# Kernel optimization log

Hardware: AMD Instinct MI355X
Metric: run time of the kernel (lower is better)

Reference implementation:

```python
import jax, jax.numpy as jnp
import numpy as np


def setup_inputs() -> dict:
    key = jax.random.key(0)
    ks = jax.random.split(key, 7)
    B, L, S, H, E, M = 4, 2048, 2048, 8, 64, 4
    return {
        "queries": jax.random.normal(ks[0], (B, L, H, E), dtype=jnp.float32),
        "keys": jax.random.normal(ks[1], (B, S, H, E), dtype=jnp.float32),
        "values": jax.random.normal(ks[2], (B, S, H, E), dtype=jnp.float32),
        "query_omegas": jax.random.normal(ks[3], (B, L, H, M), dtype=jnp.float32),
        "query_thetas": jax.random.normal(ks[4], (B, L, H, M), dtype=jnp.float32),
        "key_omegas": jax.random.normal(ks[5], (B, S, H, M), dtype=jnp.float32),
        "key_thetas": jax.random.normal(ks[6], (B, S, H, M), dtype=jnp.float32),
    }


def _rotate(x, cos, sin, signs):
    # x: (B,T,H,E) split into 4 quaternion components of size E/4
    # cos/sin: (B,T,H,M); output: (B,T,H,M,E) matching torch.cat of einsum pairs
    x0, x1, x2, x3 = jnp.split(x, 4, axis=-1)  # each (B,T,H,E/4)
    c = cos[..., None]  # (B,T,H,M,1)
    s = sin[..., None]
    (a0, b0), (a1, b1), (a2, b2), (a3, b3) = signs
    parts = [
        x0[:, :, :, None, :] * c + a0 * b0[0][:, :, :, None, :] * s if False else None
    ]
    # explicit faithful construction below
    return None


def reference(queries, keys, values, query_omegas, query_thetas, key_omegas, key_thetas):
    B, L, H, E = queries.shape
    S = keys.shape[1]
    M = query_omegas.shape[-1]

    q_pos = (jnp.arange(L, dtype=queries.dtype) / L).reshape(L, 1, 1)
    k_pos = (jnp.arange(S, dtype=keys.dtype) / S).reshape(S, 1, 1)

    Qa = query_omegas * q_pos + query_thetas  # (B,L,H,M)
    Ka = key_omegas * k_pos + key_thetas      # (B,S,H,M)
    Qc, Qs = jnp.cos(Qa)[..., None], jnp.sin(Qa)[..., None]  # (B,L,H,M,1)
    Kc, Ks = jnp.cos(Ka)[..., None], jnp.sin(Ka)[..., None]  # (B,S,H,M,1)

    q0, q1, q2, q3 = [q[:, :, :, None, :] for q in jnp.split(queries, 4, axis=-1)]  # (B,L,H,1,E/4)
    k0, k1, k2, k3 = [k[:, :, :, None, :] for k in jnp.split(keys, 4, axis=-1)]     # (B,S,H,1,E/4)

    Q_rot = jnp.concatenate([
        q0 * Qc - q1 * Qs,
        q1 * Qc + q0 * Qs,
        q2 * Qc + q3 * Qs,
        q3 * Qc - q2 * Qs,
    ], axis=-1)  # (B,L,H,M,E)
    K_rot = jnp.concatenate([
        k0 * Kc - k2 * Ks,
        k1 * Kc - k3 * Ks,
        k2 * Kc + k0 * Ks,
        k3 * Kc + k1 * Ks,
    ], axis=-1)  # (B,S,H,M,E)

    scale = 1.0 / np.sqrt(E)
    scores = jnp.einsum('blhme,bshme->bhls', Q_rot, K_rot) / M  # (B,H,L,S)
    A = jax.nn.softmax(scale * scores, axis=-1)
    V = jnp.einsum('bhls,bshd->blhd', A, values)  # (B,L,H,E)
    return V
```

## Files before the change

kernel.cpp:

```cpp
#include <hip/hip_runtime.h>
#include <math.h>


#define B_ 4
#define L_ 2048
#define S_ 2048
#define H_ 8
#define E_ 64
#define M_ 4
#define QBLK 256
#define NTH 512

typedef _Float16 f16x4 __attribute__((ext_vector_type(4)));
typedef _Float16 f16x8 __attribute__((ext_vector_type(8)));
typedef __fp16 fp16x2 __attribute__((ext_vector_type(2)));
typedef float f32x4 __attribute__((ext_vector_type(4)));

union H4U { f16x4 h; fp16x2 p[2]; };
union H8U { f16x8 h; fp16x2 p[4]; };
union F4U { float4 v; float f[4]; };

__device__ __forceinline__ f16x4 cvt4(float x, float y, float z, float w) {
    H4U r;
    r.p[0] = __builtin_amdgcn_cvt_pkrtz(x, y);
    r.p[1] = __builtin_amdgcn_cvt_pkrtz(z, w);
    return r.h;
}
__device__ __forceinline__ f16x8 cvt8(const float* v) {
    H8U r;
#pragma unroll
    for (int i = 0; i < 4; ++i) r.p[i] = __builtin_amdgcn_cvt_pkrtz(v[2 * i], v[2 * i + 1]);
    return r.h;
}

__global__ __launch_bounds__(NTH)
void qattn7(const float* __restrict__ qp, const float* __restrict__ kp,
            const float* __restrict__ vp,
            const float* __restrict__ qo, const float* __restrict__ qt,
            const float* __restrict__ ko, const float* __restrict__ ktt,
            float* __restrict__ out)
{
    const int bid0 = blockIdx.x;
    const int nl = (bid0 & 7) * 32 + (bid0 >> 3);
    const int l0 = (nl & 7) * QBLK;
    const int h  = (nl >> 3) & 7;
    const int b  = nl >> 6;
    const int t  = threadIdx.x;
    const int wv   = t >> 6;
    const int lane = t & 63;
    const int quad = lane >> 4;
    const int nn   = lane & 15;

    __shared__ __align__(16) unsigned char smem[73728];
    _Float16 (*krot)[256] = reinterpret_cast<_Float16 (*)[256]>(smem);
    _Float16 (*vts)[64]   = reinterpret_cast<_Float16 (*)[64]>(smem + 32768);
    _Float16 (*pss)[64]   = reinterpret_cast<_Float16 (*)[64]>(smem + 40960);
    float (*qstage)[64] = reinterpret_cast<float (*)[64]>(smem);
    float (*qtrc)[4] = reinterpret_cast<float (*)[4]>(smem + 65536);
    float (*qtrs)[4] = reinterpret_cast<float (*)[4]>(smem + 65536 + 4096);

    const float* kb0 = kp  + ((size_t)((b * S_) * H_ + h)) * E_;
    const float* vb0 = vp  + ((size_t)((b * S_) * H_ + h)) * E_;
    const float* kob = ko  + ((size_t)((b * S_) * H_ + h)) * M_;
    const float* ktb = ktt + ((size_t)((b * S_) * H_ + h)) * M_;

    const int key_r = t >> 3;
    const int ccr   = (t >> 1) & 3;
    const int eh    = t & 1;
    const int swz   = key_r & 7;
    const int tt = t & 255;
    const int kg = tt >> 4;
    const int eg = tt & 15;

    F4U kA[2], kB[2], omR, thR, vv[4];
    auto LOAD = [&](int s0) {
        const float* kr = kb0 + (size_t)(s0 + key_r) * (H_ * E_);
        kA[0].v = *(const float4*)(kr + ccr * 16 + eh * 8);
        kA[1].v = *(const float4*)(kr + ccr * 16 + eh * 8 + 4);
        kB[0].v = *(const float4*)(kr + (ccr ^ 2) * 16 + eh * 8);
        kB[1].v = *(const float4*)(kr + (ccr ^ 2) * 16 + eh * 8 + 4);
        omR.v = *(const float4*)(kob + (size_t)(s0 + key_r) * (H_ * M_));
        thR.v = *(const float4*)(ktb + (size_t)(s0 + key_r) * (H_ * M_));
        if (t >= 256) {
#pragma unroll
            for (int j = 0; j < 4; ++j)
                vv[j].v = *(const float4*)(vb0 + (size_t)(s0 + kg * 4 + j) * (H_ * E_) + eg * 4);
        }
    };
    LOAD(0);

    f16x8 qa[2][8];
    {
        const float* qb = qp + ((size_t)((b * L_ + l0) * H_ + h)) * E_;
#pragma unroll
        for (int i = 0; i < 8; ++i) {
            int idx = t + NTH * i;
            int row = idx >> 4, c16 = idx & 15;
            *(float4*)&qstage[row][c16 * 4] =
                *(const float4*)(qb + (size_t)row * (H_ * E_) + c16 * 4);
        }
        {
            int row = t >> 1, m0 = (t & 1) * 2;
#pragma unroll
            for (int dm = 0; dm < 2; ++dm) {
                int m = m0 + dm;
                size_t off = (size_t)((b * L_ + l0 + row) * H_ + h) * M_ + m;
                float ang = qo[off] * ((float)(l0 + row) * (1.0f / L_)) + qt[off];
                float sv, cv;
                __sincosf(ang, &sv, &cv);
                qtrc[row][m] = cv;
                qtrs[row][m] = sv;
            }
        }
        __syncthreads();
#pragma unroll
        for (int set = 0; set < 2; ++set) {
            const int row = wv * 32 + set * 16 + nn;
            const int i0 = (quad & 1) * 8;
            float sl0[8], sl1[8], sl2[8], sl3[8];
            *(float4*)&sl0[0] = *(float4*)&qstage[row][ 0 + i0];
            *(float4*)&sl0[4] = *(float4*)&qstage[row][ 4 + i0];
            *(float4*)&sl1[0] = *(float4*)&qstage[row][16 + i0];
            *(float4*)&sl1[4] = *(float4*)&qstage[row][20 + i0];
            *(float4*)&sl2[0] = *(float4*)&qstage[row][32 + i0];
            *(float4*)&sl2[4] = *(float4*)&qstage[row][36 + i0];
            *(float4*)&sl3[0] = *(float4*)&qstage[row][48 + i0];
            *(float4*)&sl3[4] = *(float4*)&qstage[row][52 + i0];
            const bool hiC = (quad & 2) != 0;
            float aE[8], bE[8], aO[8], bO[8];
#pragma unroll
            for (int j = 0; j < 8; ++j) {
                aE[j] = hiC ? sl1[j] : sl0[j];
                bE[j] = hiC ? sl0[j] : sl1[j];
                aO[j] = hiC ? sl3[j] : sl2[j];
                bO[j] = hiC ? sl2[j] : sl3[j];
            }
            F4U qc4, qs4;
            qc4.v = *(float4*)&qtrc[row][0];
            qs4.v = *(float4*)&qtrs[row][0];
            const float SC = 0.04508422017f;
#pragma unroll
            for (int m = 0; m < 4; ++m) {
                float cm = qc4.f[m] * SC;
                float sm = qs4.f[m] * SC;
                float sE = hiC ? sm : -sm;
                float vE[8], vO[8];
#pragma unroll
                for (int j = 0; j < 8; ++j) {
                    vE[j] = fmaf(bE[j], sE, aE[j] * cm);
                    vO[j] = fmaf(bO[j], -sE, aO[j] * cm);
                }
                qa[set][2 * m]     = cvt8(vE);
                qa[set][2 * m + 1] = cvt8(vO);
            }
        }
        __syncthreads();
    }

    f32x4 Oacc[2][4] = {{{0,0,0,0},{0,0,0,0},{0,0,0,0},{0,0,0,0}},
                        {{0,0,0,0},{0,0,0,0},{0,0,0,0},{0,0,0,0}}};
    float mrow[2] = {-1e30f, -1e30f};
    float lrow[2] = {0.f, 0.f};
    const int xr0 = nn & 7;
    const int swq = (nn & 7) ^ (nn >> 3);

    for (int s0 = 0; s0 < S_; s0 += 64) {
        {
            float af[8], bf[8];
#pragma unroll
            for (int i2 = 0; i2 < 4; ++i2) {
                af[i2]     = kA[0].f[i2];
                af[4 + i2] = kA[1].f[i2];
                bf[i2]     = kB[0].f[i2];
                bf[4 + i2] = kB[1].f[i2];
            }
            float posk = (float)(s0 + key_r) * (1.0f / S_);
            float kcv[4], ksv[4];
#pragma unroll
            for (int m = 0; m < 4; ++m) {
                float ang = omR.f[m] * posk + thR.f[m];
                __sincosf(ang, &ksv[m], &kcv[m]);
            }
            const float sgn = (ccr >= 2) ? 1.f : -1.f;
#pragma unroll
            for (int m = 0; m < 4; ++m) {
                float cm = kcv[m], sm = ksv[m] * sgn;
                float vals[8];
#pragma unroll
                for (int i = 0; i < 8; ++i)
                    vals[i] = fmaf(bf[i], sm, af[i] * cm);
                int ch = (m * 8) | ((ccr * 2 + eh) ^ swz);
                *(f16x8*)&krot[key_r][ch * 8] = cvt8(vals);
            }
        }
        if (t >= 256) {
#pragma unroll
            for (int e = 0; e < 4; ++e) {
                int row = eg * 4 + e;
                int ch = ((kg >> 1) ^ (row & 7));
                *(f16x4*)&vts[row][ch * 8 + (kg & 1) * 4] =
                    cvt4(vv[0].f[e], vv[1].f[e], vv[2].f[e], vv[3].f[e]);
            }
        }
        if (s0 + 64 < S_) LOAD(s0 + 64);
        __syncthreads();

        float sc[2][4][4];
#pragma unroll
        for (int kt2 = 0; kt2 < 4; ++kt2) {
            const int keyb = kt2 * 16 + nn;
            f32x4 acc0 = {0, 0, 0, 0}, acc1 = {0, 0, 0, 0};
#pragma unroll
            for (int ks = 0; ks < 8; ++ks) {
                f16x8 bK = *(const f16x8*)&krot[keyb][((ks * 4 + quad) ^ xr0) * 8];
                acc0 = __builtin_amdgcn_mfma_f32_16x16x32_f16(bK, qa[0][ks], acc0, 0, 0, 0);
                acc1 = __builtin_amdgcn_mfma_f32_16x16x32_f16(bK, qa[1][ks], acc1, 0, 0, 0);
            }
#pragma unroll
            for (int r = 0; r < 4; ++r) { sc[0][kt2][r] = acc0[r]; sc[1][kt2][r] = acc1[r]; }
        }

#pragma unroll
        for (int set = 0; set < 2; ++set) {
            const int rowq = wv * 32 + set * 16 + nn;
            float m01 = fmaxf(fmaxf(sc[set][0][0], sc[set][0][1]), fmaxf(sc[set][0][2], sc[set][0][3]));
            float m23 = fmaxf(fmaxf(sc[set][1][0], sc[set][1][1]), fmaxf(sc[set][1][2], sc[set][1][3]));
            float m45 = fmaxf(fmaxf(sc[set][2][0], sc[set][2][1]), fmaxf(sc[set][2][2], sc[set][2][3]));
            float m67 = fmaxf(fmaxf(sc[set][3][0], sc[set][3][1]), fmaxf(sc[set][3][2], sc[set][3][3]));
            float tm = fmaxf(fmaxf(m01, m23), fmaxf(m45, m67));
            tm = fmaxf(tm, __shfl_xor(tm, 16));
            tm = fmaxf(tm, __shfl_xor(tm, 32));

            if (__any(tm > mrow[set] + 8.0f)) {
                float mnew  = fmaxf(mrow[set], tm);
                float alpha = __builtin_amdgcn_exp2f(mrow[set] - mnew);
                mrow[set] = mnew;
                lrow[set] *= alpha;
#pragma unroll
                for (int r = 0; r < 4; ++r) {
                    float ar = __shfl(alpha, quad * 4 + r, 64);
                    Oacc[set][0][r] *= ar; Oacc[set][1][r] *= ar;
                    Oacc[set][2][r] *= ar; Oacc[set][3][r] *= ar;
                }
            }

            float p[4][4];
#pragma unroll
            for (int kt2 = 0; kt2 < 4; ++kt2)
#pragma unroll
                for (int r = 0; r < 4; ++r)
                    p[kt2][r] = __builtin_amdgcn_exp2f(sc[set][kt2][r] - mrow[set]);

            float s0s = (p[0][0] + p[0][1]) + (p[0][2] + p[0][3]);
            float s1s = (p[1][0] + p[1][1]) + (p[1][2] + p[1][3]);
            float s2s = (p[2][0] + p[2][1]) + (p[2][2] + p[2][3]);
            float s3s = (p[3][0] + p[3][1]) + (p[3][2] + p[3][3]);
            float psum = (s0s + s1s) + (s2s + s3s);
            psum += __shfl_xor(psum, 16);
            psum += __shfl_xor(psum, 32);
            lrow[set] += psum;

#pragma unroll
            for (int kt2 = 0; kt2 < 4; ++kt2)
#pragma unroll
                for (int d2 = 0; d2 < 2; ++d2) {
                    fp16x2 pkv = __builtin_amdgcn_cvt_pkrtz(p[kt2][2 * d2], p[kt2][2 * d2 + 1]);
                    int key0 = kt2 * 16 + quad * 4 + 2 * d2;
                    int ch = (key0 >> 3) ^ swq;
                    *(fp16x2*)&pss[rowq][ch * 8 + (key0 & 7)] = pkv;
                }
        }

        {
            const int pr0 = wv * 32 + nn;
#pragma unroll
            for (int ks2 = 0; ks2 < 2; ++ks2) {
                f16x8 pf0 = *(const f16x8*)&pss[pr0     ][((quad + 4 * ks2) ^ swq) * 8];
                f16x8 pf1 = *(const f16x8*)&pss[pr0 + 16][((quad + 4 * ks2) ^ swq) * 8];
#pragma unroll
                for (int et = 0; et < 4; ++et) {
                    int e = et * 16 + nn;
                    f16x8 vf = *(const f16x8*)&vts[e][((quad + 4 * ks2) ^ (e & 7)) * 8];
                    Oacc[0][et] = __builtin_amdgcn_mfma_f32_16x16x32_f16(pf0, vf, Oacc[0][et], 0, 0, 0);
                    Oacc[1][et] = __builtin_amdgcn_mfma_f32_16x16x32_f16(pf1, vf, Oacc[1][et], 0, 0, 0);
                }
            }
        }
        __syncthreads();
    }

    float* ob = out + ((size_t)((b * L_ + l0) * H_ + h)) * E_;
#pragma unroll
    for (int set = 0; set < 2; ++set)
#pragma unroll
        for (int r = 0; r < 4; ++r) {
            float lr = __shfl(lrow[set], quad * 4 + r, 64);
            float inv = 1.0f / lr;
            int row = wv * 32 + set * 16 + quad * 4 + r;
#pragma unroll
            for (int et = 0; et < 4; ++et)
                ob[(size_t)row * (H_ * E_) + et * 16 + nn] = Oacc[set][et][r] * inv;
        }
}

extern "C" void kernel_launch(void* const* d_in, const int* in_sizes, int n_in,
                              void* d_out, int out_size, void* d_ws, size_t ws_size,
                              hipStream_t stream) {
    const float* qp = (const float*)d_in[0];
    const float* kp = (const float*)d_in[1];
    const float* vp = (const float*)d_in[2];
    const float* qo = (const float*)d_in[3];
    const float* qt = (const float*)d_in[4];
    const float* ko = (const float*)d_in[5];
    const float* kt = (const float*)d_in[6];
    float* out = (float*)d_out;

    qattn7<<<dim3(B_ * H_ * (L_ / QBLK)), dim3(NTH), 0, stream>>>(
        qp, kp, vp, qo, qt, ko, kt, out);
}
```

Before: 196.7 us.

## Double-buffer rotated K/V tiles in LDS and overlap build with softmax

Splits the per-tile K-rotation and V-transpose into a BUILD step that writes into alternating LDS buffers. The next tile is built between the QK MFMAs and the softmax, which removes one barrier per iteration and overlaps global loads and rotation math with compute. It also uses hardware sin/cos builtins, packs P stores into 8-byte writes, and raises wave priority around the MFMA sections. LDS use grows from 72KB to 112KB per block, which could limit residency.

```diff
diff --git a/kernel.cpp b/kernel.cpp
--- a/kernel.cpp
+++ b/kernel.cpp
@@ -10,6 +10,12 @@
 #define M_ 4
 #define QBLK 256
 #define NTH 512
+#define NTILES 32
+
+#define KROT_OFF 0
+#define VTS_OFF  65536
+#define PSS_OFF  81920
+#define SMEM_BYTES 114688
 
 typedef _Float16 f16x4 __attribute__((ext_vector_type(4)));
 typedef _Float16 f16x8 __attribute__((ext_vector_type(8)));
@@ -19,6 +25,13 @@
 union H4U { f16x4 h; fp16x2 p[2]; };
 union H8U { f16x8 h; fp16x2 p[4]; };
 union F4U { float4 v; float f[4]; };
+
+#if __has_builtin(__builtin_amdgcn_sinf) && __has_builtin(__builtin_amdgcn_cosf)
+#define FSINCOS(ang, s, c) do { float _rv = (ang) * 0.15915494309189535f; \
+    (s) = __builtin_amdgcn_sinf(_rv); (c) = __builtin_amdgcn_cosf(_rv); } while (0)
+#else
+#define FSINCOS(ang, s, c) __sincosf((ang), &(s), &(c))
+#endif
 
 __device__ __forceinline__ f16x4 cvt4(float x, float y, float z, float w) {
     H4U r;
@@ -34,7 +47,7 @@
 }
 
 __global__ __launch_bounds__(NTH)
-void qattn7(const float* __restrict__ qp, const float* __restrict__ kp,
+void qattn8(const float* __restrict__ qp, const float* __restrict__ kp,
             const float* __restrict__ vp,
             const float* __restrict__ qo, const float* __restrict__ qt,
             const float* __restrict__ ko, const float* __restrict__ ktt,
@@ -51,13 +64,11 @@
     const int quad = lane >> 4;
     const int nn   = lane & 15;
 
-    __shared__ __align__(16) unsigned char smem[73728];
-    _Float16 (*krot)[256] = reinterpret_cast<_Float16 (*)[256]>(smem);
-    _Float16 (*vts)[64]   = reinterpret_cast<_Float16 (*)[64]>(smem + 32768);
-    _Float16 (*pss)[64]   = reinterpret_cast<_Float16 (*)[64]>(smem + 40960);
+    __shared__ __align__(16) unsigned char smem[SMEM_BYTES];
+    _Float16 (*pss)[64] = reinterpret_cast<_Float16 (*)[64]>(smem + PSS_OFF);
     float (*qstage)[64] = reinterpret_cast<float (*)[64]>(smem);
-    float (*qtrc)[4] = reinterpret_cast<float (*)[4]>(smem + 65536);
-    float (*qtrs)[4] = reinterpret_cast<float (*)[4]>(smem + 65536 + 4096);
+    float (*qtrc)[4] = reinterpret_cast<float (*)[4]>(smem + PSS_OFF);
+    float (*qtrs)[4] = reinterpret_cast<float (*)[4]>(smem + PSS_OFF + 4096);
 
     const float* kb0 = kp  + ((size_t)((b * S_) * H_ + h)) * E_;
     const float* vb0 = vp  + ((size_t)((b * S_) * H_ + h)) * E_;
@@ -87,6 +98,49 @@
                 vv[j].v = *(const float4*)(vb0 + (size_t)(s0 + kg * 4 + j) * (H_ * E_) + eg * 4);
         }
     };
+
+    auto BUILD = [&](int s0, int koff, int voff) {
+        _Float16 (*krw)[256] = reinterpret_cast<_Float16 (*)[256]>(smem + koff);
+        _Float16 (*vtw)[64]  = reinterpret_cast<_Float16 (*)[64]>(smem + voff);
+        {
+            float af[8], bf[8];
+#pragma unroll
+            for (int i2 = 0; i2 < 4; ++i2) {
+                af[i2]     = kA[0].f[i2];
+                af[4 + i2] = kA[1].f[i2];
+                bf[i2]     = kB[0].f[i2];
+                bf[4 + i2] = kB[1].f[i2];
+            }
+            float posk = (float)(s0 + key_r) * (1.0f / S_);
+            float kcv[4], ksv[4];
+#pragma unroll
+            for (int m = 0; m < 4; ++m) {
+                float ang = fmaf(omR.f[m], posk, thR.f[m]);
+                FSINCOS(ang, ksv[m], kcv[m]);
+            }
+            const float sgn = (ccr >= 2) ? 1.f : -1.f;
+#pragma unroll
+            for (int m = 0; m < 4; ++m) {
+                float cm = kcv[m], sm = ksv[m] * sgn;
+                float vals[8];
+#pragma unroll
+                for (int i = 0; i < 8; ++i)
+                    vals[i] = fmaf(bf[i], sm, af[i] * cm);
+                int ch = (m * 8) | ((ccr * 2 + eh) ^ swz);
+                *(f16x8*)&krw[key_r][ch * 8] = cvt8(vals);
+            }
+        }
+        if (t >= 256) {
+#pragma unroll
+            for (int e = 0; e < 4; ++e) {
+                int row = eg * 4 + e;
+                int ch = ((kg >> 1) ^ (row & 7));
+                *(f16x4*)&vtw[row][ch * 8 + (kg & 1) * 4] =
+                    cvt4(vv[0].f[e], vv[1].f[e], vv[2].f[e], vv[3].f[e]);
+            }
+        }
+    };
+
     LOAD(0);
 
     f16x8 qa[2][8];
@@ -107,7 +161,7 @@
                 size_t off = (size_t)((b * L_ + l0 + row) * H_ + h) * M_ + m;
                 float ang = qo[off] * ((float)(l0 + row) * (1.0f / L_)) + qt[off];
                 float sv, cv;
-                __sincosf(ang, &sv, &cv);
+                FSINCOS(ang, sv, cv);
                 qtrc[row][m] = cv;
                 qtrs[row][m] = sv;
             }
@@ -164,48 +218,18 @@
     const int xr0 = nn & 7;
     const int swq = (nn & 7) ^ (nn >> 3);
 
-    for (int s0 = 0; s0 < S_; s0 += 64) {
-        {
-            float af[8], bf[8];
-#pragma unroll
-            for (int i2 = 0; i2 < 4; ++i2) {
-                af[i2]     = kA[0].f[i2];
-                af[4 + i2] = kA[1].f[i2];
-                bf[i2]     = kB[0].f[i2];
-                bf[4 + i2] = kB[1].f[i2];
-            }
-            float posk = (float)(s0 + key_r) * (1.0f / S_);
-            float kcv[4], ksv[4];
-#pragma unroll
-            for (int m = 0; m < 4; ++m) {
-                float ang = omR.f[m] * posk + thR.f[m];
-                __sincosf(ang, &ksv[m], &kcv[m]);
-            }
-            const float sgn = (ccr >= 2) ? 1.f : -1.f;
-#pragma unroll
-            for (int m = 0; m < 4; ++m) {
-                float cm = kcv[m], sm = ksv[m] * sgn;
-                float vals[8];
-#pragma unroll
-                for (int i = 0; i < 8; ++i)
-                    vals[i] = fmaf(bf[i], sm, af[i] * cm);
-                int ch = (m * 8) | ((ccr * 2 + eh) ^ swz);
-                *(f16x8*)&krot[key_r][ch * 8] = cvt8(vals);
-            }
-        }
-        if (t >= 256) {
-#pragma unroll
-            for (int e = 0; e < 4; ++e) {
-                int row = eg * 4 + e;
-                int ch = ((kg >> 1) ^ (row & 7));
-                *(f16x4*)&vts[row][ch * 8 + (kg & 1) * 4] =
-                    cvt4(vv[0].f[e], vv[1].f[e], vv[2].f[e], vv[3].f[e]);
-            }
-        }
-        if (s0 + 64 < S_) LOAD(s0 + 64);
-        __syncthreads();
+    BUILD(0, KROT_OFF, VTS_OFF);
+    LOAD(64);
+    __syncthreads();
+
+    for (int ti = 0; ti < NTILES; ++ti) {
+        _Float16 (*krot)[256] = reinterpret_cast<_Float16 (*)[256]>(
+            smem + KROT_OFF + (ti & 1) * 32768);
+        _Float16 (*vts)[64] = reinterpret_cast<_Float16 (*)[64]>(
+            smem + VTS_OFF + (ti & 1) * 8192);
 
         float sc[2][4][4];
+        __builtin_amdgcn_s_setprio(1);
 #pragma unroll
         for (int kt2 = 0; kt2 < 4; ++kt2) {
             const int keyb = kt2 * 16 + nn;
@@ -218,6 +242,13 @@
             }
 #pragma unroll
             for (int r = 0; r < 4; ++r) { sc[0][kt2][r] = acc0[r]; sc[1][kt2][r] = acc1[r]; }
+        }
+        __builtin_amdgcn_s_setprio(0);
+
+        if (ti + 1 < NTILES) {
+            BUILD((ti + 1) * 64, KROT_OFF + ((ti + 1) & 1) * 32768,
+                  VTS_OFF + ((ti + 1) & 1) * 8192);
+            if (ti + 2 < NTILES) LOAD((ti + 2) * 64);
         }
 
 #pragma unroll
@@ -261,18 +292,19 @@
             lrow[set] += psum;
 
 #pragma unroll
-            for (int kt2 = 0; kt2 < 4; ++kt2)
-#pragma unroll
-                for (int d2 = 0; d2 < 2; ++d2) {
-                    fp16x2 pkv = __builtin_amdgcn_cvt_pkrtz(p[kt2][2 * d2], p[kt2][2 * d2 + 1]);
-                    int key0 = kt2 * 16 + quad * 4 + 2 * d2;
-                    int ch = (key0 >> 3) ^ swq;
-                    *(fp16x2*)&pss[rowq][ch * 8 + (key0 & 7)] = pkv;
-                }
+            for (int kt2 = 0; kt2 < 4; ++kt2) {
+                H4U pk;
+                pk.p[0] = __builtin_amdgcn_cvt_pkrtz(p[kt2][0], p[kt2][1]);
+                pk.p[1] = __builtin_amdgcn_cvt_pkrtz(p[kt2][2], p[kt2][3]);
+                int key0 = kt2 * 16 + quad * 4;
+                int ch = (key0 >> 3) ^ swq;
+                *(f16x4*)&pss[rowq][ch * 8 + (key0 & 7)] = pk.h;
+            }
         }
 
         {
             const int pr0 = wv * 32 + nn;
+            __builtin_amdgcn_s_setprio(1);
 #pragma unroll
             for (int ks2 = 0; ks2 < 2; ++ks2) {
                 f16x8 pf0 = *(const f16x8*)&pss[pr0     ][((quad + 4 * ks2) ^ swq) * 8];
@@ -285,6 +317,7 @@
                     Oacc[1][et] = __builtin_amdgcn_mfma_f32_16x16x32_f16(pf1, vf, Oacc[1][et], 0, 0, 0);
                 }
             }
+            __builtin_amdgcn_s_setprio(0);
         }
         __syncthreads();
     }
@@ -315,6 +348,6 @@
     const float* kt = (const float*)d_in[6];
     float* out = (float*)d_out;
 
-    qattn7<<<dim3(B_ * H_ * (L_ / QBLK)), dim3(NTH), 0, stream>>>(
+    qattn8<<<dim3(B_ * H_ * (L_ / QBLK)), dim3(NTH), 0, stream>>>(
         qp, kp, vp, qo, qt, ko, kt, out);
 }
```

Measured after the change: 193.0 us. About the same (-1.9%).
